# Performance work log

Hardware: AMD Instinct MI355X
Metric: run time of the kernel (lower is better)

Reference implementation:

```python
import jax, jax.numpy as jnp
import numpy as np

COMMITMENT_COST = 0.25
NUM_EMBEDDINGS = 512

def _conv(x, w, b=None, stride=1, pad=1):
    y = jax.lax.conv_general_dilated(x, w, (stride, stride), [(pad, pad)] * 2,
                                     dimension_numbers=('NCHW', 'OIHW', 'NCHW'))
    return y if b is None else y + b[None, :, None, None]

def _tconv(x, w, b, stride=2, k=4, p=1):
    # torch ConvTranspose2d(in,out,k,s,p): weight (in,out,kh,kw)
    w2 = jnp.flip(w, (2, 3)).transpose(1, 0, 2, 3)  # -> (out,in,kh,kw)
    pad = k - 1 - p
    y = jax.lax.conv_general_dilated(x, w2, (1, 1), [(pad, pad)] * 2,
                                     lhs_dilation=(stride, stride),
                                     dimension_numbers=('NCHW', 'OIHW', 'NCHW'))
    return y + b[None, :, None, None]

def _residual(x, w1, w2):
    return x + _conv(jax.nn.relu(_conv(jax.nn.relu(x), w1)), w2)

def _res_stack(x, w11, w12, w21, w22):
    x = jax.nn.relu(_residual(x, w11, w12))
    return jax.nn.relu(_residual(x, w21, w22))

def _vq(z, codebook):
    # z: (B, D, H, W) -> NHWC
    inputs = z.transpose(0, 2, 3, 1)
    B, H, W, D = inputs.shape
    flat = inputs.reshape(-1, D)  # (N, D)
    # squared euclidean distances (argmin-equivalent to torch.cdist)
    d2 = (jnp.sum(flat * flat, 1, keepdims=True)
          - 2.0 * flat @ codebook.T
          + jnp.sum(codebook * codebook, 1)[None, :])  # (N, K)
    idx = jnp.argmin(d2, axis=1)
    quantized = codebook[idx].reshape(B, H, W, D)
    sg = jax.lax.stop_gradient
    e_latent_loss = jnp.mean((sg(quantized) - inputs) ** 2)
    q_latent_loss = jnp.mean((quantized - sg(inputs)) ** 2)
    loss = q_latent_loss + COMMITMENT_COST * e_latent_loss
    quantized_st = inputs + sg(quantized - inputs)
    avg_probs = jnp.bincount(idx, length=NUM_EMBEDDINGS).astype(jnp.float32) / flat.shape[0]
    perplexity = jnp.exp(-jnp.sum(avg_probs * jnp.log(avg_probs + 1e-10)))
    return loss, quantized_st.transpose(0, 3, 1, 2), perplexity

def setup_inputs() -> dict:
    key = jax.random.key(0)
    ks = jax.random.split(key, 24)
    Hc, D, K = 128, 64, NUM_EMBEDDINGS
    s = 0.05
    rn = lambda k, sh: (jax.random.normal(k, sh, jnp.float32) * s)
    inp = {
        'x': jax.random.normal(ks[0], (32, 3, 256, 256), jnp.float32),
        # encoder
        'e1w': rn(ks[1], (Hc // 2, 3, 4, 4)), 'e1b': rn(ks[2], (Hc // 2,)),
        'e2w': rn(ks[3], (Hc, Hc // 2, 4, 4)), 'e2b': rn(ks[4], (Hc,)),
        'er11': rn(ks[5], (Hc, Hc, 3, 3)), 'er12': rn(ks[6], (Hc, Hc, 3, 3)),
        'er21': rn(ks[7], (Hc, Hc, 3, 3)), 'er22': rn(ks[8], (Hc, Hc, 3, 3)),
        # pre-vq conv 1x1
        'pvw': rn(ks[9], (D, Hc, 1, 1)), 'pvb': rn(ks[10], (D,)),
        # codebook: uniform(-1/K, 1/K)
        'cb': jax.random.uniform(ks[11], (K, D), jnp.float32, -1.0 / K, 1.0 / K),
        # decoder
        'd1w': rn(ks[12], (Hc, D, 3, 3)), 'd1b': rn(ks[13], (Hc,)),
        'dr11': rn(ks[14], (Hc, Hc, 3, 3)), 'dr12': rn(ks[15], (Hc, Hc, 3, 3)),
        'dr21': rn(ks[16], (Hc, Hc, 3, 3)), 'dr22': rn(ks[17], (Hc, Hc, 3, 3)),
        't1w': rn(ks[18], (Hc, Hc // 2, 4, 4)), 't1b': rn(ks[19], (Hc // 2,)),
        't2w': rn(ks[20], (Hc // 2, 3, 4, 4)), 't2b': rn(ks[21], (3,)),
    }
    return inp

def reference(x, e1w, e1b, e2w, e2b, er11, er12, er21, er22, pvw, pvb, cb,
              d1w, d1b, dr11, dr12, dr21, dr22, t1w, t1b, t2w, t2b):
    # encoder
    z = jax.nn.relu(_conv(x, e1w, e1b, stride=2, pad=1))
    z = _conv(z, e2w, e2b, stride=2, pad=1)
    z = _res_stack(z, er11, er12, er21, er22)
    # pre-vq 1x1 conv
    z = _conv(z, pvw, pvb, stride=1, pad=0)
    # vector quantization
    loss, quantized, perplexity = _vq(z, cb)
    # decoder
    h = _conv(quantized, d1w, d1b, stride=1, pad=1)
    h = _res_stack(h, dr11, dr12, dr21, dr22)
    h = jax.nn.relu(_tconv(h, t1w, t1b))
    x_recon = _tconv(h, t2w, t2b)
    return loss, x_recon, perplexity
```

## Files before the change

kernel.cpp:

```cpp
#include <hip/hip_runtime.h>

typedef short bf16x8 __attribute__((ext_vector_type(8)));
typedef float f32x4 __attribute__((ext_vector_type(4)));
typedef unsigned short ushort4v __attribute__((ext_vector_type(4)));
typedef unsigned int u32x4 __attribute__((ext_vector_type(4)));

__device__ __forceinline__ unsigned short f2bf(float f) {
  unsigned u = __float_as_uint(f);
  unsigned r = (u + 0x7FFFu + ((u >> 16) & 1u)) >> 16;
  return (unsigned short)r;
}
__device__ __forceinline__ float bf2f(unsigned short u) {
  return __uint_as_float(((unsigned)u) << 16);
}

__device__ __forceinline__ bf16x8 relu_bf8(bf16x8 v) {
  u32x4 u;
  __builtin_memcpy(&u, &v, 16);
  #pragma unroll
  for (int i = 0; i < 4; i++) {
    unsigned s = u[i] & 0x80008000u;
    u[i] &= ~((s >> 15) * 0xFFFFu);
  }
  bf16x8 r;
  __builtin_memcpy(&r, &u, 16);
  return r;
}

__device__ __forceinline__ int xcd_swz(int bid, int n) {
  return (bid & 7) * (n >> 3) + (bid >> 3);
}

__global__ void init_k(int* __restrict__ hist) {
  int t = threadIdx.x;
  if (t < 512) hist[t] = 0;
}

__global__ void cbh_k(const float* __restrict__ cb, float* __restrict__ cbh) {
  int k = blockIdx.x * 256 + threadIdx.x;
  if (k >= 512) return;
  const float* c = cb + k * 64;
  float s = 0.f;
  #pragma unroll
  for (int d = 0; d < 64; d++) s = fmaf(c[d], c[d], s);
  cbh[k] = 0.5f * s;
}

__global__ void repack_cbf_k(const float* __restrict__ cb,
                             unsigned short* __restrict__ cbf) {
  int idx = blockIdx.x * 256 + threadIdx.x;
  if (idx >= 32768) return;
  int j = idx & 7;
  int lane = (idx >> 3) & 63;
  int ks = (idx >> 9) & 1;
  int m = idx >> 10;
  int code = m * 16 + (lane & 15);
  int d = ks * 32 + (lane >> 4) * 8 + j;
  cbf[idx] = f2bf(cb[code * 64 + d]);
}

template <int CIN>
__global__ void repack_frag_k(const float* __restrict__ w,
                              unsigned short* __restrict__ wf) {
  int idx = blockIdx.x * 256 + threadIdx.x;
  int total = (CIN / 32) * 9 * 8 * 512;
  if (idx >= total) return;
  int j = idx & 7;
  int lane = (idx >> 3) & 63;
  int M = (idx >> 9) & 7;
  int tk = idx >> 12;
  int tap = tk % 9;
  int kstep = tk / 9;
  int co = M * 16 + (lane & 15);
  int ci = kstep * 32 + (lane >> 4) * 8 + j;
  wf[idx] = f2bf(w[((size_t)co * CIN + ci) * 9 + tap]);
}

__global__ void repack_e1f_k(const float* __restrict__ w,
                             unsigned short* __restrict__ wf) {
  int idx = blockIdx.x * 256 + threadIdx.x;
  if (idx >= 4096) return;
  int j = idx & 7;
  int lane = (idx >> 3) & 63;
  int m = (idx >> 9) & 3;
  int ks = idx >> 11;
  int co = m * 16 + (lane & 15);
  int k = ks * 32 + (lane >> 4) * 8 + j;
  float v = (k < 48) ? w[co * 48 + k] : 0.f;
  wf[idx] = f2bf(v);
}

__global__ void repack_e2f_k(const float* __restrict__ w,
                             unsigned short* __restrict__ wf) {
  int idx = blockIdx.x * 256 + threadIdx.x;
  if (idx >= 131072) return;
  int j = idx & 7;
  int lane = (idx >> 3) & 63;
  int M = (idx >> 9) & 7;
  int tap = (idx >> 12) & 15;
  int ks = idx >> 16;
  int co = M * 16 + (lane & 15);
  int ci = ks * 32 + (lane >> 4) * 8 + j;
  wf[idx] = f2bf(w[((size_t)co * 64 + ci) * 16 + tap]);
}

__global__ void repack_pvf_k(const float* __restrict__ w,
                             unsigned short* __restrict__ wf) {
  int idx = blockIdx.x * 256 + threadIdx.x;
  if (idx >= 8192) return;
  int j = idx & 7;
  int lane = (idx >> 3) & 63;
  int m = (idx >> 9) & 3;
  int ks = idx >> 11;
  int co = m * 16 + (lane & 15);
  int ci = ks * 32 + (lane >> 4) * 8 + j;
  wf[idx] = f2bf(w[co * 128 + ci]);
}

__global__ void repack_t1f_k(const float* __restrict__ w,
                             unsigned short* __restrict__ wf) {
  int idx = blockIdx.x * 256 + threadIdx.x;
  if (idx >= 131072) return;
  int j = idx & 7;
  int lane = (idx >> 3) & 63;
  int m = (idx >> 9) & 3;
  int tap = (idx >> 11) & 3;
  int ks = (idx >> 13) & 3;
  int par = (idx >> 15) & 3;
  int sy = par >> 1, sx = par & 1;
  int ty = tap >> 1, tx = tap & 1;
  int ky = sy ? (ty ? 0 : 2) : (ty ? 1 : 3);
  int kx = sx ? (tx ? 0 : 2) : (tx ? 1 : 3);
  int co = m * 16 + (lane & 15);
  int ci = ks * 32 + (lane >> 4) * 8 + j;
  wf[idx] = f2bf(w[((size_t)ci * 64 + co) * 16 + ky * 4 + kx]);
}

__global__ void repack_t2f_k(const float* __restrict__ w,
                             unsigned short* __restrict__ wf) {
  int idx = blockIdx.x * 256 + threadIdx.x;
  if (idx >= 16384) return;
  int j = idx & 7;
  int lane = (idx >> 3) & 63;
  int tap = (idx >> 9) & 3;
  int ks = (idx >> 11) & 1;
  int par = idx >> 12;
  int sy = par >> 1, sx = par & 1;
  int ty = tap >> 1, tx = tap & 1;
  int ky = sy ? (ty ? 0 : 2) : (ty ? 1 : 3);
  int kx = sx ? (tx ? 0 : 2) : (tx ? 1 : 3);
  int co = lane & 15;
  int ci = ks * 32 + (lane >> 4) * 8 + j;
  float v = (co < 3) ? w[((size_t)ci * 3 + co) * 16 + ky * 4 + kx] : 0.f;
  wf[idx] = f2bf(v);
}

__global__ __launch_bounds__(256, 4) void e1m_k(
    const float* __restrict__ x, const unsigned short* __restrict__ wf,
    const float* __restrict__ bias, unsigned short* __restrict__ out) {
  __shared__ unsigned short patch[128 * 72];
  int blk = xcd_swz(blockIdx.x, gridDim.x);
  int b = blk >> 7;
  int oy = blk & 127;
  int t = threadIdx.x;
  int w = t >> 6, l = t & 63;
  int cib = (l >> 4) * 8, colb = l & 15;
  const float* xb = x + (size_t)b * 3 * 65536;
  {
    int p = t & 127;
    int kb = (t >> 7) * 32;
    int px2 = 2 * p - 1;
    int oy2 = 2 * oy - 1;
    bf16x8 pk[4];
    #pragma unroll
    for (int c = 0; c < 4; c++) {
      #pragma unroll
      for (int j = 0; j < 8; j++) {
        int k = kb + c * 8 + j;
        float v = 0.f;
        if (k < 48) {
          int ci = k >> 4;
          int ky = (k >> 2) & 3, kx = k & 3;
          int iy = oy2 + ky, ix = px2 + kx;
          if ((unsigned)iy < 256u && (unsigned)ix < 256u)
            v = xb[ci * 65536 + iy * 256 + ix];
        }
        pk[c][j] = (short)f2bf(v);
      }
    }
    unsigned short* row = &patch[p * 72 + kb];
    #pragma unroll
    for (int c = 0; c < 4; c++)
      *(bf16x8*)&row[c * 8] = pk[c];
  }
  __syncthreads();
  f32x4 acc[8];
  #pragma unroll
  for (int n = 0; n < 8; n++) acc[n] = (f32x4){0.f, 0.f, 0.f, 0.f};
  #pragma unroll
  for (int ks = 0; ks < 2; ks++) {
    bf16x8 af = *(const bf16x8*)&wf[((size_t)(ks * 4 + w) * 64 + l) * 8];
    #pragma unroll
    for (int n = 0; n < 8; n++) {
      bf16x8 bfrag =
          *(const bf16x8*)&patch[(n * 16 + colb) * 72 + ks * 32 + cib];
      acc[n] = __builtin_amdgcn_mfma_f32_16x16x32_bf16(af, bfrag, acc[n],
                                                       0, 0, 0);
    }
  }
  int cob = w * 16 + (l >> 4) * 4;
  f32x4 bj = *(const f32x4*)&bias[cob];
  #pragma unroll
  for (int n = 0; n < 8; n++) {
    int p = n * 16 + colb;
    ushort4v pk = {f2bf(fmaxf(acc[n][0] + bj[0], 0.f)),
                   f2bf(fmaxf(acc[n][1] + bj[1], 0.f)),
                   f2bf(fmaxf(acc[n][2] + bj[2], 0.f)),
                   f2bf(fmaxf(acc[n][3] + bj[3], 0.f))};
    *(ushort4v*)&out[((size_t)b * 16384 + oy * 128 + p) * 64 + cob] = pk;
  }
}

__global__ __launch_bounds__(256, 4) void e2m_k(
    const unsigned short* __restrict__ in,
    const unsigned short* __restrict__ wf, const float* __restrict__ bias,
    unsigned short* __restrict__ out) {
  __shared__ unsigned short patch[528 * 32];
  int blk = xcd_swz(blockIdx.x, gridDim.x);
  int b = blk >> 6;
  int oy = blk & 63;
  int t = threadIdx.x;
  int w = t >> 6, l = t & 63;
  int qr = l >> 4, colb = l & 15;
  f32x4 acc[2][4];
  #pragma unroll
  for (int m = 0; m < 2; m++)
    #pragma unroll
    for (int n = 0; n < 4; n++) acc[m][n] = (f32x4){0.f, 0.f, 0.f, 0.f};
  const unsigned short* inb = in + (size_t)b * 16384 * 64;
  for (int ks = 0; ks < 2; ks++) {
    __syncthreads();
    for (int j = 0; j < 9; j++) {
      int base_chunk = j * 256 + w * 64;
      if (base_chunk >= 2112) break;
      int chunk = base_chunk + l;
      int pos = chunk >> 2, qs = chunk & 3;
      int r = pos / 132, s2 = pos - r * 132;
      int cr = (s2 < 66) ? (2 * s2) : (2 * (s2 - 66) + 1);
      int iy = 2 * oy - 1 + r, ix = cr - 1;
      int qg = qs ^ ((pos >> 1) & 3);
      if ((unsigned)iy < 128u && (unsigned)ix < 128u) {
        __builtin_amdgcn_global_load_lds(
            (const __attribute__((address_space(1))) unsigned int*)(const void*)
                &inb[((size_t)iy * 128 + ix) * 64 + ks * 32 + qg * 8],
            (__attribute__((address_space(3))) unsigned int*)(void*)
                &patch[(size_t)base_chunk * 8],
            16, 0, 0);
      } else {
        *(bf16x8*)&patch[chunk * 8] = (bf16x8){0, 0, 0, 0, 0, 0, 0, 0};
      }
    }
    __syncthreads();
    __builtin_amdgcn_s_setprio(1);
    #pragma unroll
    for (int tap = 0; tap < 16; tap++) {
      int ky = tap >> 2, kx = tap & 3;
      bf16x8 bfrag[4];
      #pragma unroll
      for (int n = 0; n < 4; n++) {
        int ox = n * 16 + colb;
        int pos = ky * 132 + (kx & 1) * 66 + ox + (kx >> 1);
        int qsl = qr ^ ((pos >> 1) & 3);
        bfrag[n] = *(const bf16x8*)&patch[pos * 32 + qsl * 8];
      }
      const unsigned short* wft = wf + ((size_t)(ks * 16 + tap) * 8) * 512;
      #pragma unroll
      for (int m = 0; m < 2; m++) {
        bf16x8 af = *(const bf16x8*)&wft[((w * 2 + m) * 64 + l) * 8];
        #pragma unroll
        for (int n = 0; n < 4; n++)
          acc[m][n] = __builtin_amdgcn_mfma_f32_16x16x32_bf16(af, bfrag[n],
                                                              acc[m][n], 0, 0, 0);
      }
    }
    __builtin_amdgcn_s_setprio(0);
  }
  #pragma unroll
  for (int m = 0; m < 2; m++) {
    int cob = (w * 2 + m) * 16 + qr * 4;
    f32x4 bj = *(const f32x4*)&bias[cob];
    #pragma unroll
    for (int n = 0; n < 4; n++) {
      int ox = n * 16 + colb;
      size_t adr = ((size_t)(b * 4096 + oy * 64 + ox)) * 128 + cob;
      ushort4v pre = {f2bf(acc[m][n][0] + bj[0]), f2bf(acc[m][n][1] + bj[1]),
                      f2bf(acc[m][n][2] + bj[2]), f2bf(acc[m][n][3] + bj[3])};
      *(ushort4v*)&out[adr] = pre;
    }
  }
}

template <int CIN, bool RES_ADD, bool RELU_IN, bool HAS_BIAS, bool PRE_ONLY>
__global__ __launch_bounds__(256, 4) void conv3nh_k(
    const unsigned short* __restrict__ in,
    const unsigned short* __restrict__ wf,
    const float* __restrict__ bias,
    const unsigned short* __restrict__ res,
    unsigned short* __restrict__ out) {
  constexpr int KO = CIN / 64;
  __shared__ unsigned short patch[2 * 264 * 36];
  int blk = xcd_swz(blockIdx.x, gridDim.x);
  int b = blk >> 5;
  int tile = blk & 31;
  int y0 = tile * 2;
  int t = threadIdx.x;
  int w = t >> 6, l = t & 63;
  int wm = w >> 1, wn = w & 1;
  int n0 = wn * 64;
  int cib = (l >> 4) * 8, colb = l & 15;
  f32x4 acc[4][4];
  #pragma unroll
  for (int m = 0; m < 4; m++)
    #pragma unroll
    for (int n = 0; n < 4; n++) acc[m][n] = (f32x4){0.f, 0.f, 0.f, 0.f};
  const unsigned short* inb = in + (size_t)b * 4096 * CIN;
  for (int ko = 0; ko < KO; ko++) {
    __syncthreads();
    for (int idx = t; idx < 2112; idx += 256) {
      int q = idx & 7;
      int pos = idx >> 3;
      int r = pos / 66, c = pos - r * 66;
      int y = y0 - 1 + r, x = c - 1;
      bf16x8 v = (bf16x8){0, 0, 0, 0, 0, 0, 0, 0};
      if ((unsigned)y < 64u && (unsigned)x < 64u)
        v = *(const bf16x8*)&inb[((size_t)(y * 64 + x)) * CIN + ko * 64 + q * 8];
      if (RELU_IN) v = relu_bf8(v);
      int ksi = q >> 2, qq = q & 3;
      *(bf16x8*)&patch[ksi * 9504 + pos * 36 + qq * 8] = v;
    }
    __syncthreads();
    __builtin_amdgcn_s_setprio(1);
    #pragma unroll
    for (int tap = 0; tap < 9; tap++) {
      int ky = tap / 3, kx = tap % 3;
      #pragma unroll
      for (int ksi = 0; ksi < 2; ksi++) {
        bf16x8 bfrag[4];
        #pragma unroll
        for (int n = 0; n < 4; n++) {
          int p = n0 + n * 16 + colb;
          int pr = p >> 6, pc = p & 63;
          int pos = (pr + ky) * 66 + (pc + kx);
          bfrag[n] = *(const bf16x8*)&patch[ksi * 9504 + pos * 36 + cib];
        }
        const unsigned short* wft =
            wf + (size_t)(ko * 2 + ksi) * 9 * 4096 + (size_t)tap * 4096;
        bf16x8 afrag[4];
        #pragma unroll
        for (int m = 0; m < 4; m++)
          afrag[m] = *(const bf16x8*)&wft[((wm * 4 + m) * 64 + l) * 8];
        #pragma unroll
        for (int m = 0; m < 4; m++)
          #pragma unroll
          for (int n = 0; n < 4; n++)
            acc[m][n] = __builtin_amdgcn_mfma_f32_16x16x32_bf16(
                afrag[m], bfrag[n], acc[m][n], 0, 0, 0);
      }
    }
    __builtin_amdgcn_s_setprio(0);
  }
  #pragma unroll
  for (int m = 0; m < 4; m++) {
    int cobase = wm * 64 + m * 16 + (l >> 4) * 4;
    float b0 = HAS_BIAS ? bias[cobase] : 0.f;
    float b1 = HAS_BIAS ? bias[cobase + 1] : 0.f;
    float b2 = HAS_BIAS ? bias[cobase + 2] : 0.f;
    float b3 = HAS_BIAS ? bias[cobase + 3] : 0.f;
    #pragma unroll
    for (int n = 0; n < 4; n++) {
      int p = n0 + n * 16 + colb;
      size_t adr = ((size_t)(b * 4096 + tile * 128 + p)) * 128 + cobase;
      float f0 = acc[m][n][0] + b0, f1 = acc[m][n][1] + b1;
      float f2 = acc[m][n][2] + b2, f3 = acc[m][n][3] + b3;
      if (RES_ADD) {
        ushort4v rv = *(const ushort4v*)&res[adr];
        f0 += bf2f(rv.x); f1 += bf2f(rv.y); f2 += bf2f(rv.z); f3 += bf2f(rv.w);
      }
      ushort4v pk;
      if (PRE_ONLY) {
        pk.x = f2bf(f0); pk.y = f2bf(f1); pk.z = f2bf(f2); pk.w = f2bf(f3);
      } else {
        pk.x = f2bf(fmaxf(f0, 0.f)); pk.y = f2bf(fmaxf(f1, 0.f));
        pk.z = f2bf(fmaxf(f2, 0.f)); pk.w = f2bf(fmaxf(f3, 0.f));
      }
      *(ushort4v*)&out[adr] = pk;
    }
  }
}

__global__ __launch_bounds__(256, 2) void vqf_k(
    const unsigned short* __restrict__ in,
    const unsigned short* __restrict__ wf, const float* __restrict__ bias,
    const unsigned short* __restrict__ cbf, const float* __restrict__ cbh,
    const float* __restrict__ cb,
    unsigned short* __restrict__ q,
    unsigned short* __restrict__ bidx,
    float* __restrict__ part, int part_off) {
  __shared__ unsigned short zt[256 * 72];
  __shared__ unsigned short bidx_s[256];
  __shared__ float red[256];
  int blk = blockIdx.x;
  int b = blk >> 4;
  int hw0 = (blk & 15) * 256;
  int t = threadIdx.x;
  int w = t >> 6, l = t & 63;
  int n0 = w * 64;
  int cib = (l >> 4) * 8, colb = l & 15;
  {
    f32x4 acc[4][4];
    #pragma unroll
    for (int m = 0; m < 4; m++)
      #pragma unroll
      for (int n = 0; n < 4; n++) acc[m][n] = (f32x4){0.f, 0.f, 0.f, 0.f};
    const unsigned short* inb = in + ((size_t)(b * 4096 + hw0)) * 128;
    for (int ks = 0; ks < 4; ks++) {
      bf16x8 bfrag[4];
      #pragma unroll
      for (int n = 0; n < 4; n++) {
        int p = n0 + n * 16 + colb;
        bfrag[n] = *(const bf16x8*)&inb[(size_t)p * 128 + ks * 32 + cib];
      }
      const unsigned short* wk = wf + ks * 4 * 512;
      #pragma unroll
      for (int m = 0; m < 4; m++) {
        bf16x8 af = *(const bf16x8*)&wk[(m * 64 + l) * 8];
        #pragma unroll
        for (int n = 0; n < 4; n++)
          acc[m][n] = __builtin_amdgcn_mfma_f32_16x16x32_bf16(af, bfrag[n],
                                                              acc[m][n], 0, 0, 0);
      }
    }
    #pragma unroll
    for (int m = 0; m < 4; m++) {
      int d0 = m * 16 + (l >> 4) * 4;
      f32x4 bj = *(const f32x4*)&bias[d0];
      #pragma unroll
      for (int n = 0; n < 4; n++) {
        int p = n0 + n * 16 + colb;
        ushort4v pk = {f2bf(acc[m][n][0] + bj[0]), f2bf(acc[m][n][1] + bj[1]),
                       f2bf(acc[m][n][2] + bj[2]), f2bf(acc[m][n][3] + bj[3])};
        *(ushort4v*)&zt[p * 72 + d0] = pk;
      }
    }
  }
  __syncthreads();
  {
    bf16x8 zfrag[4][2];
    #pragma unroll
    for (int n = 0; n < 4; n++) {
      int p = n0 + n * 16 + colb;
      #pragma unroll
      for (int k2 = 0; k2 < 2; k2++)
        zfrag[n][k2] = *(const bf16x8*)&zt[p * 72 + k2 * 32 + cib];
    }
    float best[4];
    int bid[4];
    #pragma unroll
    for (int n = 0; n < 4; n++) { best[n] = -1e30f; bid[n] = 0; }
    for (int m = 0; m < 32; m++) {
      bf16x8 a0 = *(const bf16x8*)&cbf[((size_t)(m * 2 + 0) * 64 + l) * 8];
      bf16x8 a1 = *(const bf16x8*)&cbf[((size_t)(m * 2 + 1) * 64 + l) * 8];
      int code0 = m * 16 + (l >> 4) * 4;
      f32x4 ch = *(const f32x4*)&cbh[code0];
      #pragma unroll
      for (int n = 0; n < 4; n++) {
        f32x4 acc2 = (f32x4){0.f, 0.f, 0.f, 0.f};
        acc2 = __builtin_amdgcn_mfma_f32_16x16x32_bf16(a0, zfrag[n][0], acc2, 0, 0, 0);
        acc2 = __builtin_amdgcn_mfma_f32_16x16x32_bf16(a1, zfrag[n][1], acc2, 0, 0, 0);
        #pragma unroll
        for (int r = 0; r < 4; r++) {
          float sc = acc2[r] - ch[r];
          if (sc > best[n]) { best[n] = sc; bid[n] = code0 + r; }
        }
      }
    }
    #pragma unroll
    for (int n = 0; n < 4; n++) {
      #pragma unroll
      for (int off = 16; off <= 32; off <<= 1) {
        float ob = __shfl_xor(best[n], off, 64);
        int oi = __shfl_xor(bid[n], off, 64);
        if (ob > best[n] || (ob == best[n] && oi < bid[n])) {
          best[n] = ob;
          bid[n] = oi;
        }
      }
      if ((l >> 4) == 0) bidx_s[n0 + n * 16 + colb] = (unsigned short)bid[n];
    }
  }
  __syncthreads();
  int bi = bidx_s[t];
  bidx[(size_t)b * 4096 + hw0 + t] = (unsigned short)bi;
  {
    const float* cq = cb + bi * 64;
    unsigned short* qp = q + ((size_t)(b * 4096 + hw0 + t)) * 64;
    const unsigned short* zp = &zt[t * 72];
    float ls = 0.f;
    #pragma unroll
    for (int g = 0; g < 8; g++) {
      u32x4 zv = *(const u32x4*)&zp[g * 8];
      u32x4 qv;
      #pragma unroll
      for (int h = 0; h < 4; h++) {
        int d = g * 8 + h * 2;
        float q0 = cq[d], q1 = cq[d + 1];
        float z0 = __uint_as_float(zv[h] << 16);
        float z1 = __uint_as_float(zv[h] & 0xFFFF0000u);
        float d0 = q0 - z0, d1 = q1 - z1;
        ls = fmaf(d0, d0, ls);
        ls = fmaf(d1, d1, ls);
        qv[h] = (unsigned)f2bf(q0) | ((unsigned)f2bf(q1) << 16);
      }
      *(u32x4*)&qp[g * 8] = qv;
    }
    red[t] = ls;
    __syncthreads();
    for (int s = 128; s > 0; s >>= 1) {
      if (t < s) red[t] += red[t + s];
      __syncthreads();
    }
    if (t == 0) part[part_off + blk] = red[0];
  }
}

__global__ __launch_bounds__(1024) void vq_hist_k(
    const unsigned short* __restrict__ bidx, int* __restrict__ hist) {
  __shared__ int hl[512];
  int t = threadIdx.x;
  if (t < 512) hl[t] = 0;
  __syncthreads();
  int base = blockIdx.x * 16384;
  for (int i = t; i < 16384; i += 1024)
    atomicAdd(&hl[bidx[base + i]], 1);
  __syncthreads();
  if (t < 512 && hl[t] > 0) atomicAdd(&hist[t], hl[t]);
}

__global__ __launch_bounds__(256, 2) void t1m_k(
    const unsigned short* __restrict__ in,
    const unsigned short* __restrict__ wf, const float* __restrict__ bias,
    unsigned short* __restrict__ out) {
  __shared__ unsigned short patch[264 * 36];
  int blk = xcd_swz(blockIdx.x, gridDim.x);
  int b = blk >> 5;
  int a0 = (blk & 31) * 2;
  int t = threadIdx.x;
  int w = t >> 6, l = t & 63;
  int sy = w >> 1, sx = w & 1;
  int cib = (l >> 4) * 8, colb = l & 15;
  f32x4 acc[4][8];
  #pragma unroll
  for (int m = 0; m < 4; m++)
    #pragma unroll
    for (int n = 0; n < 8; n++) acc[m][n] = (f32x4){0.f, 0.f, 0.f, 0.f};
  const unsigned short* inb = in + (size_t)b * 4096 * 128;
  for (int ks = 0; ks < 4; ks++) {
    __syncthreads();
    for (int idx = t; idx < 1056; idx += 256) {
      int q = idx & 3;
      int pos = idx >> 2;
      int r = pos / 66, c = pos - r * 66;
      int y = a0 - 1 + r, x = c - 1;
      bf16x8 v = (bf16x8){0, 0, 0, 0, 0, 0, 0, 0};
      if ((unsigned)y < 64u && (unsigned)x < 64u)
        v = *(const bf16x8*)&inb[((size_t)(y * 64 + x)) * 128 + ks * 32 + q * 8];
      *(bf16x8*)&patch[pos * 36 + q * 8] = v;
    }
    __syncthreads();
    __builtin_amdgcn_s_setprio(1);
    const unsigned short* wpar = wf + (size_t)((sy * 2 + sx) * 4 + ks) * 8192;
    #pragma unroll
    for (int tap = 0; tap < 4; tap++) {
      int ty = tap >> 1, tx = tap & 1;
      int d = sy ? ty + 1 : ty;
      int e = sx ? tx + 1 : tx;
      bf16x8 bfrag[8];
      #pragma unroll
      for (int n = 0; n < 8; n++) {
        int p = n * 16 + colb;
        int ar = p >> 6, pc = p & 63;
        int pos = (ar + d) * 66 + (pc + e);
        bfrag[n] = *(const bf16x8*)&patch[pos * 36 + cib];
      }
      bf16x8 afrag[4];
      #pragma unroll
      for (int m = 0; m < 4; m++)
        afrag[m] = *(const bf16x8*)&wpar[(tap * 256 + m * 64 + l) * 8];
      #pragma unroll
      for (int m = 0; m < 4; m++)
        #pragma unroll
        for (int n = 0; n < 8; n++)
          acc[m][n] = __builtin_amdgcn_mfma_f32_16x16x32_bf16(
              afrag[m], bfrag[n], acc[m][n], 0, 0, 0);
    }
    __builtin_amdgcn_s_setprio(0);
  }
  #pragma unroll
  for (int m = 0; m < 4; m++) {
    int cob = m * 16 + (l >> 4) * 4;
    float b0 = bias[cob], b1 = bias[cob + 1], b2 = bias[cob + 2],
          b3 = bias[cob + 3];
    #pragma unroll
    for (int n = 0; n < 8; n++) {
      int p = n * 16 + colb;
      int ar = p >> 6, pc = p & 63;
      int oy = 2 * (a0 + ar) + sy, ox = 2 * pc + sx;
      ushort4v pk;
      pk.x = f2bf(fmaxf(acc[m][n][0] + b0, 0.f));
      pk.y = f2bf(fmaxf(acc[m][n][1] + b1, 0.f));
      pk.z = f2bf(fmaxf(acc[m][n][2] + b2, 0.f));
      pk.w = f2bf(fmaxf(acc[m][n][3] + b3, 0.f));
      *(ushort4v*)&out[((size_t)b * 16384 + oy * 128 + ox) * 64 + cob] = pk;
    }
  }
}

__global__ __launch_bounds__(256, 2) void t2m_k(
    const unsigned short* __restrict__ in,
    const unsigned short* __restrict__ wf,
    const float* __restrict__ bias, float* __restrict__ out) {
  __shared__ unsigned short patch[528 * 36];
  int blk = xcd_swz(blockIdx.x, gridDim.x);
  int b = blk >> 6;
  int a0 = (blk & 63) * 2;
  int t = threadIdx.x;
  int w = t >> 6, l = t & 63;
  int sy = w >> 1, sx = w & 1;
  int cib = (l >> 4) * 8, colb = l & 15;
  f32x4 acc[2][8];
  #pragma unroll
  for (int ar = 0; ar < 2; ar++)
    #pragma unroll
    for (int n = 0; n < 8; n++) acc[ar][n] = (f32x4){0.f, 0.f, 0.f, 0.f};
  bf16x8 af[2][4];
  #pragma unroll
  for (int ks = 0; ks < 2; ks++) {
    const unsigned short* wpar = wf + (size_t)((sy * 2 + sx) * 2 + ks) * 2048;
    #pragma unroll
    for (int tap = 0; tap < 4; tap++)
      af[ks][tap] = *(const bf16x8*)&wpar[(tap * 64 + l) * 8];
  }
  const unsigned short* inb = in + (size_t)b * 16384 * 64;
  for (int ks = 0; ks < 2; ks++) {
    __syncthreads();
    for (int idx = t; idx < 2112; idx += 256) {
      int q = idx & 3;
      int pos = idx >> 2;
      int r = pos / 132, c = pos - r * 132;
      int y = a0 - 1 + r, x = c - 1;
      bf16x8 v = (bf16x8){0, 0, 0, 0, 0, 0, 0, 0};
      if ((unsigned)y < 128u && (unsigned)x < 128u)
        v = *(const bf16x8*)&inb[((size_t)(y * 128 + x)) * 64 + ks * 32 + q * 8];
      *(bf16x8*)&patch[pos * 36 + q * 8] = v;
    }
    __syncthreads();
    __builtin_amdgcn_s_setprio(1);
    #pragma unroll
    for (int tap = 0; tap < 4; tap++) {
      int ty = tap >> 1, tx = tap & 1;
      int d = sy ? ty + 1 : ty;
      int e = sx ? tx + 1 : tx;
      #pragma unroll
      for (int ar = 0; ar < 2; ar++) {
        #pragma unroll
        for (int n = 0; n < 8; n++) {
          int pc = n * 16 + colb;
          int pos = (ar + d) * 132 + (pc + e);
          bf16x8 bfrag = *(const bf16x8*)&patch[pos * 36 + cib];
          acc[ar][n] = __builtin_amdgcn_mfma_f32_16x16x32_bf16(
              af[ks][tap], bfrag, acc[ar][n], 0, 0, 0);
        }
      }
    }
    __builtin_amdgcn_s_setprio(0);
  }
  int rb = (l >> 4) * 4;
  #pragma unroll
  for (int r = 0; r < 4; r++) {
    int co = rb + r;
    if (co < 3) {
      float bj = bias[co];
      #pragma unroll
      for (int ar = 0; ar < 2; ar++) {
        int oy = 2 * (a0 + ar) + sy;
        #pragma unroll
        for (int n = 0; n < 8; n++) {
          int pc = n * 16 + colb;
          int ox = 2 * pc + sx;
          out[((size_t)(b * 3 + co)) * 65536 + oy * 256 + ox] = acc[ar][n][r] + bj;
        }
      }
    }
  }
}

__global__ __launch_bounds__(512) void fin_k(
    const float* __restrict__ part, const int* __restrict__ hist,
    float* __restrict__ loss_out, float* __restrict__ perp_out) {
  __shared__ float red[512];
  int t = threadIdx.x;
  red[t] = part[t];
  __syncthreads();
  for (int s = 256; s > 0; s >>= 1) {
    if (t < s) red[t] += red[t + s];
    __syncthreads();
  }
  float loss = 1.25f * red[0] / 8388608.f;
  __syncthreads();
  float p = (float)hist[t] / 131072.f;
  red[t] = -p * logf(p + 1e-10f);
  __syncthreads();
  for (int s = 256; s > 0; s >>= 1) {
    if (t < s) red[t] += red[t + s];
    __syncthreads();
  }
  if (t == 0) {
    *loss_out = loss;
    *perp_out = expf(red[0]);
  }
}

extern "C" void kernel_launch(void* const* d_in, const int* in_sizes, int n_in,
                              void* d_out, int out_size, void* d_ws, size_t ws_size,
                              hipStream_t stream) {
  (void)in_sizes; (void)n_in; (void)out_size;
  const float* x    = (const float*)d_in[0];
  const float* e1w  = (const float*)d_in[1];
  const float* e1b  = (const float*)d_in[2];
  const float* e2w  = (const float*)d_in[3];
  const float* e2b  = (const float*)d_in[4];
  const float* er11 = (const float*)d_in[5];
  const float* er12 = (const float*)d_in[6];
  const float* er21 = (const float*)d_in[7];
  const float* er22 = (const float*)d_in[8];
  const float* pvw  = (const float*)d_in[9];
  const float* pvb  = (const float*)d_in[10];
  const float* cb   = (const float*)d_in[11];
  const float* d1w  = (const float*)d_in[12];
  const float* d1b  = (const float*)d_in[13];
  const float* dr11 = (const float*)d_in[14];
  const float* dr12 = (const float*)d_in[15];
  const float* dr21 = (const float*)d_in[16];
  const float* dr22 = (const float*)d_in[17];
  const float* t1w  = (const float*)d_in[18];
  const float* t1b  = (const float*)d_in[19];
  const float* t2w  = (const float*)d_in[20];
  const float* t2b  = (const float*)d_in[21];
  float* out = (float*)d_out;

  const size_t W_PVF  = 0;
  const size_t W_E2F  = W_PVF + 4096;
  const size_t W_T1F  = W_E2F + 65536;
  const size_t W_T2F  = W_T1F + 65536;
  const size_t W_D1F  = W_T2F + 8192;
  const size_t W_CBF  = W_D1F + 36864;
  const size_t W_E1F  = W_CBF + 16384;
  const size_t W_RT   = W_E1F + 2048;
  const size_t W_CBH  = W_RT + 8 * 73728;
  const size_t W_PART = W_CBH + 512;
  const size_t W_BIDX = W_PART + 512;
  const size_t W_HIST = W_BIDX + 65536;
  const size_t W_TOT  = W_HIST + 512;

  float* ws = (float*)d_ws;
  unsigned short* pvf = (unsigned short*)(ws + W_PVF);
  unsigned short* e2f = (unsigned short*)(ws + W_E2F);
  unsigned short* t1f = (unsigned short*)(ws + W_T1F);
  unsigned short* t2f = (unsigned short*)(ws + W_T2F);
  unsigned short* d1f = (unsigned short*)(ws + W_D1F);
  unsigned short* cbf = (unsigned short*)(ws + W_CBF);
  unsigned short* e1f = (unsigned short*)(ws + W_E1F);
  unsigned short* rtf[8];
  for (int i = 0; i < 8; i++)
    rtf[i] = (unsigned short*)(ws + W_RT + (size_t)i * 73728);
  float* cbh  = ws + W_CBH;
  float* part = ws + W_PART;
  unsigned short* bidx = (unsigned short*)(ws + W_BIDX);
  int*   hist = (int*)(ws + W_HIST);

  size_t wfloats = ws_size / sizeof(float);
  int BC = 32;
  while (BC > 1 && W_TOT + (size_t)BC * 1572864 > wfloats) BC >>= 1;
  int nchunk = 32 / BC;

  unsigned short* E1  = (unsigned short*)(ws + W_TOT);
  unsigned short* P1  = (unsigned short*)(ws + W_TOT + (size_t)BC * 524288);
  unsigned short* P2  = P1 + (size_t)BC * 524288;
  unsigned short* P4  = P2 + (size_t)BC * 524288;
  unsigned short* Zbf = P4 + (size_t)BC * 524288;
  unsigned short* Qbf = Zbf + (size_t)BC * 262144;

  init_k<<<1, 512, 0, stream>>>(hist);
  cbh_k<<<2, 256, 0, stream>>>(cb, cbh);
  repack_cbf_k<<<128, 256, 0, stream>>>(cb, cbf);

  repack_e1f_k<<<16, 256, 0, stream>>>(e1w, e1f);
  repack_pvf_k<<<32, 256, 0, stream>>>(pvw, pvf);
  repack_e2f_k<<<512, 256, 0, stream>>>(e2w, e2f);
  repack_t1f_k<<<512, 256, 0, stream>>>(t1w, t1f);
  repack_t2f_k<<<64, 256, 0, stream>>>(t2w, t2f);
  repack_frag_k<64><<<288, 256, 0, stream>>>(d1w, d1f);
  repack_frag_k<128><<<576, 256, 0, stream>>>(er11, rtf[0]);
  repack_frag_k<128><<<576, 256, 0, stream>>>(er12, rtf[1]);
  repack_frag_k<128><<<576, 256, 0, stream>>>(er21, rtf[2]);
  repack_frag_k<128><<<576, 256, 0, stream>>>(er22, rtf[3]);
  repack_frag_k<128><<<576, 256, 0, stream>>>(dr11, rtf[4]);
  repack_frag_k<128><<<576, 256, 0, stream>>>(dr12, rtf[5]);
  repack_frag_k<128><<<576, 256, 0, stream>>>(dr21, rtf[6]);
  repack_frag_k<128><<<576, 256, 0, stream>>>(dr22, rtf[7]);

  for (int c = 0; c < nchunk; ++c) {
    const float* xc = x + (size_t)c * BC * 3 * 65536;
    float* outc = out + 1 + (size_t)c * BC * 3 * 65536;
    unsigned short* bidxc = bidx + (size_t)c * BC * 4096;
    e1m_k<<<BC * 128, 256, 0, stream>>>(xc, e1f, e1b, E1);
    e2m_k<<<BC * 64, 256, 0, stream>>>(E1, e2f, e2b, P1);
    conv3nh_k<128, false, true,  false, false><<<BC * 32, 256, 0, stream>>>(P1, rtf[0], nullptr, nullptr, P4);
    conv3nh_k<128, true,  false, false, false><<<BC * 32, 256, 0, stream>>>(P4, rtf[1], nullptr, P1, P2);
    conv3nh_k<128, false, false, false, false><<<BC * 32, 256, 0, stream>>>(P2, rtf[2], nullptr, nullptr, P4);
    conv3nh_k<128, true,  false, false, false><<<BC * 32, 256, 0, stream>>>(P4, rtf[3], nullptr, P2, P1);
    vqf_k<<<BC * 16, 256, 0, stream>>>(P1, pvf, pvb, cbf, cbh, cb, Qbf, bidxc,
                                       part, c * BC * 16);
    conv3nh_k<64,  false, false, true,  true ><<<BC * 32, 256, 0, stream>>>(Qbf, d1f, d1b, nullptr, P1);
    conv3nh_k<128, false, true,  false, false><<<BC * 32, 256, 0, stream>>>(P1, rtf[4], nullptr, nullptr, P4);
    conv3nh_k<128, true,  false, false, false><<<BC * 32, 256, 0, stream>>>(P4, rtf[5], nullptr, P1, P2);
    conv3nh_k<128, false, false, false, false><<<BC * 32, 256, 0, stream>>>(P2, rtf[6], nullptr, nullptr, P4);
    conv3nh_k<128, true,  false, false, false><<<BC * 32, 256, 0, stream>>>(P4, rtf[7], nullptr, P2, P1);
    t1m_k<<<BC * 32, 256, 0, stream>>>(P1, t1f, t1b, E1);
    t2m_k<<<BC * 64, 256, 0, stream>>>(E1, t2f, t2b, outc);
  }
  vq_hist_k<<<8, 1024, 0, stream>>>(bidx, hist);
  fin_k<<<1, 512, 0, stream>>>(part, hist, out, out + 1 + 6291456);
}
```

Baseline: 607.2 us.

## Stage conv patches with direct global-to-LDS loads and XOR-swizzled layout

Replaces register-staged patch loading in the 3x3 conv (non-ReLU variant) and both transposed-conv kernels with global_load_lds direct-to-LDS transfers. The padded 36-element rows give way to a dense layout with an XOR swizzle on the channel chunk, which is meant to avoid bank conflicts on fragment reads. This cuts VGPR staging and instruction overhead in the load phase. The ReLU-input conv keeps register staging but adopts the swizzled layout. The risk is correctness of the lane-to-address mapping for global_load_lds and the out-of-bounds zero-fill mixing.

```diff
diff --git a/kernel.cpp b/kernel.cpp
--- a/kernel.cpp
+++ b/kernel.cpp
@@ -308,7 +308,7 @@
     const unsigned short* __restrict__ res,
     unsigned short* __restrict__ out) {
   constexpr int KO = CIN / 64;
-  __shared__ unsigned short patch[2 * 264 * 36];
+  __shared__ unsigned short patch[2112 * 8];
   int blk = xcd_swz(blockIdx.x, gridDim.x);
   int b = blk >> 5;
   int tile = blk & 31;
@@ -317,7 +317,7 @@
   int w = t >> 6, l = t & 63;
   int wm = w >> 1, wn = w & 1;
   int n0 = wn * 64;
-  int cib = (l >> 4) * 8, colb = l & 15;
+  int qr = l >> 4, colb = l & 15;
   f32x4 acc[4][4];
   #pragma unroll
   for (int m = 0; m < 4; m++)
@@ -326,17 +326,38 @@
   const unsigned short* inb = in + (size_t)b * 4096 * CIN;
   for (int ko = 0; ko < KO; ko++) {
     __syncthreads();
-    for (int idx = t; idx < 2112; idx += 256) {
-      int q = idx & 7;
-      int pos = idx >> 3;
-      int r = pos / 66, c = pos - r * 66;
-      int y = y0 - 1 + r, x = c - 1;
-      bf16x8 v = (bf16x8){0, 0, 0, 0, 0, 0, 0, 0};
-      if ((unsigned)y < 64u && (unsigned)x < 64u)
-        v = *(const bf16x8*)&inb[((size_t)(y * 64 + x)) * CIN + ko * 64 + q * 8];
-      if (RELU_IN) v = relu_bf8(v);
-      int ksi = q >> 2, qq = q & 3;
-      *(bf16x8*)&patch[ksi * 9504 + pos * 36 + qq * 8] = v;
+    if (!RELU_IN) {
+      for (int j = 0; j < 9; j++) {
+        int base_chunk = j * 256 + w * 64;
+        if (base_chunk >= 2112) break;
+        int chunk = base_chunk + l;
+        int pos = chunk >> 3, qs = chunk & 7;
+        int r = pos / 66, c = pos - r * 66;
+        int y = y0 - 1 + r, x = c - 1;
+        int qg = qs ^ (pos & 7);
+        if ((unsigned)y < 64u && (unsigned)x < 64u) {
+          __builtin_amdgcn_global_load_lds(
+              (const __attribute__((address_space(1))) unsigned int*)(const void*)
+                  &inb[((size_t)(y * 64 + x)) * CIN + ko * 64 + qg * 8],
+              (__attribute__((address_space(3))) unsigned int*)(void*)
+                  &patch[(size_t)base_chunk * 8],
+              16, 0, 0);
+        } else {
+          *(bf16x8*)&patch[chunk * 8] = (bf16x8){0, 0, 0, 0, 0, 0, 0, 0};
+        }
+      }
+    } else {
+      for (int idx = t; idx < 2112; idx += 256) {
+        int pos = idx >> 3, qs = idx & 7;
+        int r = pos / 66, c = pos - r * 66;
+        int y = y0 - 1 + r, x = c - 1;
+        int qg = qs ^ (pos & 7);
+        bf16x8 v = (bf16x8){0, 0, 0, 0, 0, 0, 0, 0};
+        if ((unsigned)y < 64u && (unsigned)x < 64u)
+          v = *(const bf16x8*)&inb[((size_t)(y * 64 + x)) * CIN + ko * 64 + qg * 8];
+        v = relu_bf8(v);
+        *(bf16x8*)&patch[idx * 8] = v;
+      }
     }
     __syncthreads();
     __builtin_amdgcn_s_setprio(1);
@@ -351,7 +372,8 @@
           int p = n0 + n * 16 + colb;
           int pr = p >> 6, pc = p & 63;
           int pos = (pr + ky) * 66 + (pc + kx);
-          bfrag[n] = *(const bf16x8*)&patch[ksi * 9504 + pos * 36 + cib];
+          int slot = (ksi * 4 + qr) ^ (pos & 7);
+          bfrag[n] = *(const bf16x8*)&patch[(pos * 8 + slot) * 8];
         }
         const unsigned short* wft =
             wf + (size_t)(ko * 2 + ksi) * 9 * 4096 + (size_t)tap * 4096;
@@ -550,14 +572,14 @@
     const unsigned short* __restrict__ in,
     const unsigned short* __restrict__ wf, const float* __restrict__ bias,
     unsigned short* __restrict__ out) {
-  __shared__ unsigned short patch[264 * 36];
+  __shared__ unsigned short patch[1088 * 8];
   int blk = xcd_swz(blockIdx.x, gridDim.x);
   int b = blk >> 5;
   int a0 = (blk & 31) * 2;
   int t = threadIdx.x;
   int w = t >> 6, l = t & 63;
   int sy = w >> 1, sx = w & 1;
-  int cib = (l >> 4) * 8, colb = l & 15;
+  int qr = l >> 4, colb = l & 15;
   f32x4 acc[4][8];
   #pragma unroll
   for (int m = 0; m < 4; m++)
@@ -566,15 +588,24 @@
   const unsigned short* inb = in + (size_t)b * 4096 * 128;
   for (int ks = 0; ks < 4; ks++) {
     __syncthreads();
-    for (int idx = t; idx < 1056; idx += 256) {
-      int q = idx & 3;
-      int pos = idx >> 2;
+    for (int j = 0; j < 5; j++) {
+      int base_chunk = j * 256 + w * 64;
+      if (base_chunk >= 1088) break;
+      int chunk = base_chunk + l;
+      int pos = chunk >> 2, qs = chunk & 3;
       int r = pos / 66, c = pos - r * 66;
       int y = a0 - 1 + r, x = c - 1;
-      bf16x8 v = (bf16x8){0, 0, 0, 0, 0, 0, 0, 0};
-      if ((unsigned)y < 64u && (unsigned)x < 64u)
-        v = *(const bf16x8*)&inb[((size_t)(y * 64 + x)) * 128 + ks * 32 + q * 8];
-      *(bf16x8*)&patch[pos * 36 + q * 8] = v;
+      int qg = qs ^ ((pos >> 1) & 3);
+      if (pos < 264 && (unsigned)y < 64u && (unsigned)x < 64u) {
+        __builtin_amdgcn_global_load_lds(
+            (const __attribute__((address_space(1))) unsigned int*)(const void*)
+                &inb[((size_t)(y * 64 + x)) * 128 + ks * 32 + qg * 8],
+            (__attribute__((address_space(3))) unsigned int*)(void*)
+                &patch[(size_t)base_chunk * 8],
+            16, 0, 0);
+      } else {
+        *(bf16x8*)&patch[chunk * 8] = (bf16x8){0, 0, 0, 0, 0, 0, 0, 0};
+      }
     }
     __syncthreads();
     __builtin_amdgcn_s_setprio(1);
@@ -590,7 +621,8 @@
         int p = n * 16 + colb;
         int ar = p >> 6, pc = p & 63;
         int pos = (ar + d) * 66 + (pc + e);
-        bfrag[n] = *(const bf16x8*)&patch[pos * 36 + cib];
+        int qsl = qr ^ ((pos >> 1) & 3);
+        bfrag[n] = *(const bf16x8*)&patch[pos * 32 + qsl * 8];
       }
       bf16x8 afrag[4];
       #pragma unroll
@@ -629,14 +661,14 @@
     const unsigned short* __restrict__ in,
     const unsigned short* __restrict__ wf,
     const float* __restrict__ bias, float* __restrict__ out) {
-  __shared__ unsigned short patch[528 * 36];
+  __shared__ unsigned short patch[2112 * 8];
   int blk = xcd_swz(blockIdx.x, gridDim.x);
   int b = blk >> 6;
   int a0 = (blk & 63) * 2;
   int t = threadIdx.x;
   int w = t >> 6, l = t & 63;
   int sy = w >> 1, sx = w & 1;
-  int cib = (l >> 4) * 8, colb = l & 15;
+  int qr = l >> 4, colb = l & 15;
   f32x4 acc[2][8];
   #pragma unroll
   for (int ar = 0; ar < 2; ar++)
@@ -653,15 +685,24 @@
   const unsigned short* inb = in + (size_t)b * 16384 * 64;
   for (int ks = 0; ks < 2; ks++) {
     __syncthreads();
-    for (int idx = t; idx < 2112; idx += 256) {
-      int q = idx & 3;
-      int pos = idx >> 2;
+    for (int j = 0; j < 9; j++) {
+      int base_chunk = j * 256 + w * 64;
+      if (base_chunk >= 2112) break;
+      int chunk = base_chunk + l;
+      int pos = chunk >> 2, qs = chunk & 3;
       int r = pos / 132, c = pos - r * 132;
       int y = a0 - 1 + r, x = c - 1;
-      bf16x8 v = (bf16x8){0, 0, 0, 0, 0, 0, 0, 0};
-      if ((unsigned)y < 128u && (unsigned)x < 128u)
-        v = *(const bf16x8*)&inb[((size_t)(y * 128 + x)) * 64 + ks * 32 + q * 8];
-      *(bf16x8*)&patch[pos * 36 + q * 8] = v;
+      int qg = qs ^ ((pos >> 1) & 3);
+      if ((unsigned)y < 128u && (unsigned)x < 128u) {
+        __builtin_amdgcn_global_load_lds(
+            (const __attribute__((address_space(1))) unsigned int*)(const void*)
+                &inb[((size_t)(y * 128 + x)) * 64 + ks * 32 + qg * 8],
+            (__attribute__((address_space(3))) unsigned int*)(void*)
+                &patch[(size_t)base_chunk * 8],
+            16, 0, 0);
+      } else {
+        *(bf16x8*)&patch[chunk * 8] = (bf16x8){0, 0, 0, 0, 0, 0, 0, 0};
+      }
     }
     __syncthreads();
     __builtin_amdgcn_s_setprio(1);
@@ -676,7 +717,8 @@
         for (int n = 0; n < 8; n++) {
           int pc = n * 16 + colb;
           int pos = (ar + d) * 132 + (pc + e);
-          bf16x8 bfrag = *(const bf16x8*)&patch[pos * 36 + cib];
+          int qsl = qr ^ ((pos >> 1) & 3);
+          bf16x8 bfrag = *(const bf16x8*)&patch[pos * 32 + qsl * 8];
           acc[ar][n] = __builtin_amdgcn_mfma_f32_16x16x32_bf16(
               af[ks][tap], bfrag, acc[ar][n], 0, 0, 0);
         }
```

Result: slower. 754.9 us (+24.3%).
